# Performance work log

Measured on AMD Instinct MI355X. Metric: run time of the kernel, lower is better.

The kernel has to match this reference:

```python
import jax, jax.numpy as jnp
import numpy as np

B = 32768        # batch
S = 256          # subnet_num
H1, H2 = 10, 6   # subnet_arch
L2_SMOOTH = 1e-3
EPS = 1e-10


def setup_inputs() -> dict:
    key = jax.random.key(0)
    k = jax.random.split(key, 7)
    def glorot(kk, shape, fan_in, fan_out):
        return (jax.random.normal(kk, shape, jnp.float32)
                * np.float32(np.sqrt(2.0 / (fan_in + fan_out))))
    x = jax.random.normal(k[0], (B, S), jnp.float32)
    W1 = glorot(k[1], (S, 1, H1), 1, H1)
    b1 = jnp.zeros((S, H1), jnp.float32)
    W2 = glorot(k[2], (S, H1, H2), H1, H2)
    b2 = jnp.zeros((S, H2), jnp.float32)
    W3 = glorot(k[3], (S, H2, 1), H2, 1)
    b3 = jnp.zeros((S, 1), jnp.float32)
    return {"x": x, "W1": W1, "b1": b1, "W2": W2, "b2": b2, "W3": W3, "b3": b3}


def _mlp_scalar(xs, W1, b1, W2, b2, W3, b3):
    # xs: scalar input of one subnet for one sample
    h = jnp.tanh(xs * W1[0] + b1)   # [H1]
    h = jnp.tanh(h @ W2 + b2)       # [H2]
    return (h @ W3 + b3)[0]         # scalar


def _per_subnet(fn):
    # inner vmap over batch (x axis 0, params broadcast), outer over subnets
    inner = jax.vmap(fn, in_axes=(0, None, None, None, None, None, None))
    return jax.vmap(inner, in_axes=(1, 0, 0, 0, 0, 0, 0))  # -> [S, B]


def reference(x, W1, b1, W2, b2, W3, b3):
    out = _per_subnet(_mlp_scalar)(x, W1, b1, W2, b2, W3, b3)           # [S, B]
    d2f = jax.grad(jax.grad(_mlp_scalar))                               # Hessian diag (scalar input)
    g2 = _per_subnet(d2f)(x, W1, b1, W2, b2, W3, b3)                    # [S, B]
    # training-mode batch stats (population std, as tf.math.reduce_std)
    mean = jnp.mean(out, axis=1, keepdims=True)                         # [S, 1]
    std = jnp.maximum(jnp.std(out, axis=1, keepdims=True), EPS)         # [S, 1]
    out_bn = ((out - mean) / std).T                                     # [B, S]
    smooth_loss = L2_SMOOTH * jnp.sum(jnp.mean(g2 * g2, axis=1) / std[:, 0])
    return out_bn, smooth_loss
```

## Files before the change

kernel.cpp:

```cpp
#include <hip/hip_runtime.h>
#include <math.h>

#define B 32768
#define S 256
#define H1 10
#define H2 6
#define ROWS 512
#define CH (B / ROWS)
#define WPB 2
#define L2_SMOOTH 1e-3f
#define EPS 1e-10f

#define LSC 2.8853900817779268f
#define C2L 0.6931471805599453f
#define RLS 0.34657359027997264f

typedef __attribute__((ext_vector_type(2))) float v2f;

__device__ __forceinline__ int rfl_i(int x) { return __builtin_amdgcn_readfirstlane(x); }
__device__ __forceinline__ float rfl(float x) {
    return __int_as_float(__builtin_amdgcn_readfirstlane(__float_as_int(x)));
}

__device__ __forceinline__ void tanh_pair_s(float a_s, float& th, float& s2) {
    const float e = __builtin_amdgcn_exp2f(a_s);
    const float r = __builtin_amdgcn_rcpf(e + 1.0f);
    th = fmaf(-2.0f, r, 1.0f);
    s2 = (4.0f * r) * (1.0f - r);
}

__global__ __launch_bounds__(128, 2) void k1_mlp(
    const float* __restrict__ x,
    const float* __restrict__ W1, const float* __restrict__ b1,
    const float* __restrict__ W2, const float* __restrict__ b2,
    const float* __restrict__ W3, const float* __restrict__ b3,
    float* __restrict__ out,
    float* __restrict__ psum,
    float* __restrict__ psum2,
    float* __restrict__ pg2)
{
    const int t   = threadIdx.x;
    const int wid = blockIdx.x * WPB + rfl_i(t >> 6);
    const int l   = t & 63;
    const int s   = wid & (S - 1);
    const int c   = wid >> 8;

    float w1[H1], w1e[H1], b1e[H1], m2w1[H1];
#pragma unroll
    for (int i = 0; i < H1; ++i) {
        const float w = rfl(W1[s * H1 + i]);
        w1[i]   = w;
        w1e[i]  = w * LSC;
        m2w1[i] = -2.0f * w * w;
        b1e[i]  = rfl(b1[s * H1 + i]) * LSC;
        asm("" : "+v"(b1e[i]));
    }
    v2f w2p[H1][3];
#pragma unroll
    for (int i = 0; i < H1; ++i)
#pragma unroll
        for (int jp = 0; jp < 3; ++jp) {
            w2p[i][jp].x = rfl(W2[(s * H1 + i) * H2 + 2 * jp    ]) * LSC;
            w2p[i][jp].y = rfl(W2[(s * H1 + i) * H2 + 2 * jp + 1]) * LSC;
        }
    v2f b2p[3];
#pragma unroll
    for (int jp = 0; jp < 3; ++jp) {
        b2p[jp].x = rfl(b2[s * H2 + 2 * jp    ]) * LSC;
        b2p[jp].y = rfl(b2[s * H2 + 2 * jp + 1]) * LSC;
    }
    float w3s[H2], w3g[H2];
#pragma unroll
    for (int j = 0; j < H2; ++j) {
        const float w = rfl(W3[s * H2 + j]);
        w3s[j] = w;
        w3g[j] = w * RLS;
    }
    float bb3 = b3[s];
    asm("" : "+v"(bb3));

    const size_t base = (size_t)(c * ROWS) * S + s + (size_t)l * S;
    const float* px = x   + base;
    float*       po = out + base;

    float so = 0.0f, so2 = 0.0f, sg2 = 0.0f;

#pragma unroll 1
    for (int k = 0; k < ROWS / 128; ++k) {
        const float xA = px[(size_t)(k * 128)      * S];
        const float xB = px[(size_t)(k * 128 + 64) * S];

        v2f vA[3], vpA[3], vppA[3], vB[3], vpB[3], vppB[3];

        float hA, tA, hB, tB;
        {
            tanh_pair_s(fmaf(xA, w1e[0], b1e[0]), hA, tA);
            tanh_pair_s(fmaf(xB, w1e[0], b1e[0]), hB, tB);
            const float hpA = tA * w1[0], hppA = (hA * hpA) * m2w1[0];
            const float hpB = tB * w1[0], hppB = (hB * hpB) * m2w1[0];
#pragma unroll
            for (int jp = 0; jp < 3; ++jp) {
                vA[jp]   = hA   * w2p[0][jp] + b2p[jp];
                vpA[jp]  = hpA  * w2p[0][jp];
                vppA[jp] = hppA * w2p[0][jp];
                vB[jp]   = hB   * w2p[0][jp] + b2p[jp];
                vpB[jp]  = hpB  * w2p[0][jp];
                vppB[jp] = hppB * w2p[0][jp];
            }
        }
#pragma unroll
        for (int i = 1; i < H1; ++i) {
            tanh_pair_s(fmaf(xA, w1e[i], b1e[i]), hA, tA);
            tanh_pair_s(fmaf(xB, w1e[i], b1e[i]), hB, tB);
            const float hpA = tA * w1[i], hppA = (hA * hpA) * m2w1[i];
            const float hpB = tB * w1[i], hppB = (hB * hpB) * m2w1[i];
#pragma unroll
            for (int jp = 0; jp < 3; ++jp) {
                vA[jp]   = hA   * w2p[i][jp] + vA[jp];
                vpA[jp]  = hpA  * w2p[i][jp] + vpA[jp];
                vppA[jp] = hppA * w2p[i][jp] + vppA[jp];
                vB[jp]   = hB   * w2p[i][jp] + vB[jp];
                vpB[jp]  = hpB  * w2p[i][jp] + vpB[jp];
                vppB[jp] = hppB * w2p[i][jp] + vppB[jp];
            }
        }

        float oA = bb3, g2A = 0.0f, oB = bb3, g2B = 0.0f;
#pragma unroll
        for (int jp = 0; jp < 3; ++jp) {
            {   float g, tg; tanh_pair_s(vA[jp].x, g, tg);
                const float q = g * vpA[jp].x, cc = -C2L * q;
                const float gpp = tg * fmaf(cc, vpA[jp].x, vppA[jp].x);
                oA = fmaf(g, w3s[2*jp], oA); g2A = fmaf(w3g[2*jp], gpp, g2A); }
            {   float g, tg; tanh_pair_s(vA[jp].y, g, tg);
                const float q = g * vpA[jp].y, cc = -C2L * q;
                const float gpp = tg * fmaf(cc, vpA[jp].y, vppA[jp].y);
                oA = fmaf(g, w3s[2*jp+1], oA); g2A = fmaf(w3g[2*jp+1], gpp, g2A); }
            {   float g, tg; tanh_pair_s(vB[jp].x, g, tg);
                const float q = g * vpB[jp].x, cc = -C2L * q;
                const float gpp = tg * fmaf(cc, vpB[jp].x, vppB[jp].x);
                oB = fmaf(g, w3s[2*jp], oB); g2B = fmaf(w3g[2*jp], gpp, g2B); }
            {   float g, tg; tanh_pair_s(vB[jp].y, g, tg);
                const float q = g * vpB[jp].y, cc = -C2L * q;
                const float gpp = tg * fmaf(cc, vpB[jp].y, vppB[jp].y);
                oB = fmaf(g, w3s[2*jp+1], oB); g2B = fmaf(w3g[2*jp+1], gpp, g2B); }
        }

        po[(size_t)(k * 128)      * S] = oA;
        po[(size_t)(k * 128 + 64) * S] = oB;
        so += oA; so2 = fmaf(oA, oA, so2); sg2 = fmaf(g2A, g2A, sg2);
        so += oB; so2 = fmaf(oB, oB, so2); sg2 = fmaf(g2B, g2B, sg2);
    }

#pragma unroll
    for (int m = 1; m < 64; m <<= 1) {
        so  += __shfl_xor(so,  m, 64);
        so2 += __shfl_xor(so2, m, 64);
        sg2 += __shfl_xor(sg2, m, 64);
    }
    if (l == 0) {
        psum [s * CH + c] = so;
        psum2[s * CH + c] = so2;
        pg2  [s * CH + c] = sg2;
    }
}

__global__ __launch_bounds__(64) void k2_reduce(
    const float* __restrict__ psum, const float* __restrict__ psum2,
    const float* __restrict__ pg2,
    float* __restrict__ mean_arr, float* __restrict__ rstd_arr,
    float* __restrict__ smooth_arr)
{
    const int s = blockIdx.x;
    const int l = threadIdx.x;

    float a  = psum [s * CH + l];
    float b_ = psum2[s * CH + l];
    float cc = pg2  [s * CH + l];
#pragma unroll
    for (int m = 1; m < 64; m <<= 1) {
        a  += __shfl_xor(a,  m, 64);
        b_ += __shfl_xor(b_, m, 64);
        cc += __shfl_xor(cc, m, 64);
    }
    if (l == 0) {
        const float inv_b = 1.0f / (float)B;
        const float mean  = a * inv_b;
        float var = b_ * inv_b - mean * mean;
        var = fmaxf(var, 0.0f);
        const float stdv = fmaxf(sqrtf(var), EPS);
        const float rstd = 1.0f / stdv;
        mean_arr[s]   = mean;
        rstd_arr[s]   = rstd;
        smooth_arr[s] = (cc * inv_b) * rstd;
    }
}

#define K3_NORM_BLOCKS (B * S / (256 * 4))
__global__ __launch_bounds__(256) void k3_norm(
    float* __restrict__ out,
    const float* __restrict__ mean_arr, const float* __restrict__ rstd_arr,
    const float* __restrict__ smooth_arr)
{
    if ((int)blockIdx.x == K3_NORM_BLOCKS) {
        const int t = threadIdx.x;
        __shared__ float sa[256];
        sa[t] = smooth_arr[t];
        __syncthreads();
        for (int st = 128; st > 0; st >>= 1) {
            if (t < st) sa[t] += sa[t + st];
            __syncthreads();
        }
        if (t == 0) out[B * S] = L2_SMOOTH * sa[0];
        return;
    }

    const int i4   = (int)blockIdx.x * 256 + (int)threadIdx.x;
    const int base = i4 * 4;
    float4 v = *reinterpret_cast<float4*>(&out[base]);
    const int s0 = base & (S - 1);
    v.x = (v.x - mean_arr[s0 + 0]) * rstd_arr[s0 + 0];
    v.y = (v.y - mean_arr[s0 + 1]) * rstd_arr[s0 + 1];
    v.z = (v.z - mean_arr[s0 + 2]) * rstd_arr[s0 + 2];
    v.w = (v.w - mean_arr[s0 + 3]) * rstd_arr[s0 + 3];
    *reinterpret_cast<float4*>(&out[base]) = v;
}

extern "C" void kernel_launch(void* const* d_in, const int* in_sizes, int n_in,
                              void* d_out, int out_size, void* d_ws, size_t ws_size,
                              hipStream_t stream) {
    const float* x  = (const float*)d_in[0];
    const float* W1 = (const float*)d_in[1];
    const float* b1 = (const float*)d_in[2];
    const float* W2 = (const float*)d_in[3];
    const float* b2 = (const float*)d_in[4];
    const float* W3 = (const float*)d_in[5];
    const float* b3 = (const float*)d_in[6];
    float* out = (float*)d_out;

    float* psum   = (float*)d_ws;
    float* psum2  = psum  + S * CH;
    float* pg2    = psum2 + S * CH;
    float* meanA  = pg2   + S * CH;
    float* rstdA  = meanA + S;
    float* smooth = rstdA + S;

    k1_mlp<<<S * CH / WPB, 64 * WPB, 0, stream>>>(
        x, W1, b1, W2, b2, W3, b3, out, psum, psum2, pg2);
    k2_reduce<<<S, 64, 0, stream>>>(psum, psum2, pg2, meanA, rstdA, smooth);
    k3_norm<<<K3_NORM_BLOCKS + 1, 256, 0, stream>>>(out, meanA, rstdA, smooth);
}
```

Baseline: 122.6 us.

## Process one sample per iteration, raise occupancy and swizzle block order

The MLP kernel now evaluates one sample per loop iteration instead of two interleaved ones. This removes the duplicated register state and lets launch bounds rise from 128 threads with 2 blocks to 256 threads with 6 blocks. Block indices are swizzled so that neighbouring blocks spread across chunks and subnets, which changes the memory access pattern and how work maps to CUs. The cost is less instruction-level parallelism per wave, which the higher wave count is meant to hide.

```diff
diff --git a/kernel.cpp b/kernel.cpp
--- a/kernel.cpp
+++ b/kernel.cpp
@@ -7,7 +7,8 @@
 #define H2 6
 #define ROWS 512
 #define CH (B / ROWS)
-#define WPB 2
+#define WPB 4
+#define NBLK (S * CH / WPB)
 #define L2_SMOOTH 1e-3f
 #define EPS 1e-10f
 
@@ -29,7 +30,7 @@
     s2 = (4.0f * r) * (1.0f - r);
 }
 
-__global__ __launch_bounds__(128, 2) void k1_mlp(
+__global__ __launch_bounds__(256, 6) void k1_mlp(
     const float* __restrict__ x,
     const float* __restrict__ W1, const float* __restrict__ b1,
     const float* __restrict__ W2, const float* __restrict__ b2,
@@ -40,7 +41,9 @@
     float* __restrict__ pg2)
 {
     const int t   = threadIdx.x;
-    const int wid = blockIdx.x * WPB + rfl_i(t >> 6);
+    const int bid = (int)blockIdx.x;
+    const int swz = (bid & 7) * (NBLK / 8) + (bid >> 3);
+    const int wid = swz * WPB + rfl_i(t >> 6);
     const int l   = t & 63;
     const int s   = wid & (S - 1);
     const int c   = wid >> 8;
@@ -68,6 +71,8 @@
     for (int jp = 0; jp < 3; ++jp) {
         b2p[jp].x = rfl(b2[s * H2 + 2 * jp    ]) * LSC;
         b2p[jp].y = rfl(b2[s * H2 + 2 * jp + 1]) * LSC;
+        asm("" : "+v"(b2p[jp].x));
+        asm("" : "+v"(b2p[jp].y));
     }
     float w3s[H2], w3g[H2];
 #pragma unroll
@@ -79,77 +84,60 @@
     float bb3 = b3[s];
     asm("" : "+v"(bb3));
 
-    const size_t base = (size_t)(c * ROWS) * S + s + (size_t)l * S;
+    const size_t base = (size_t)(c * ROWS + l) * S + s;
     const float* px = x   + base;
     float*       po = out + base;
 
     float so = 0.0f, so2 = 0.0f, sg2 = 0.0f;
 
 #pragma unroll 1
-    for (int k = 0; k < ROWS / 128; ++k) {
-        const float xA = px[(size_t)(k * 128)      * S];
-        const float xB = px[(size_t)(k * 128 + 64) * S];
-
-        v2f vA[3], vpA[3], vppA[3], vB[3], vpB[3], vppB[3];
-
-        float hA, tA, hB, tB;
+    for (int k = 0; k < ROWS / 64; ++k) {
+        const float xs = px[(size_t)(k * 64) * S];
+
+        v2f v[3], vp[3], vpp[3];
         {
-            tanh_pair_s(fmaf(xA, w1e[0], b1e[0]), hA, tA);
-            tanh_pair_s(fmaf(xB, w1e[0], b1e[0]), hB, tB);
-            const float hpA = tA * w1[0], hppA = (hA * hpA) * m2w1[0];
-            const float hpB = tB * w1[0], hppB = (hB * hpB) * m2w1[0];
+            float h, tt;
+            tanh_pair_s(fmaf(xs, w1e[0], b1e[0]), h, tt);
+            const float hp  = tt * w1[0];
+            const float hpp = (h * hp) * m2w1[0];
 #pragma unroll
             for (int jp = 0; jp < 3; ++jp) {
-                vA[jp]   = hA   * w2p[0][jp] + b2p[jp];
-                vpA[jp]  = hpA  * w2p[0][jp];
-                vppA[jp] = hppA * w2p[0][jp];
-                vB[jp]   = hB   * w2p[0][jp] + b2p[jp];
-                vpB[jp]  = hpB  * w2p[0][jp];
-                vppB[jp] = hppB * w2p[0][jp];
+                v[jp]   = h   * w2p[0][jp] + b2p[jp];
+                vp[jp]  = hp  * w2p[0][jp];
+                vpp[jp] = hpp * w2p[0][jp];
             }
         }
 #pragma unroll
         for (int i = 1; i < H1; ++i) {
-            tanh_pair_s(fmaf(xA, w1e[i], b1e[i]), hA, tA);
-            tanh_pair_s(fmaf(xB, w1e[i], b1e[i]), hB, tB);
-            const float hpA = tA * w1[i], hppA = (hA * hpA) * m2w1[i];
-            const float hpB = tB * w1[i], hppB = (hB * hpB) * m2w1[i];
+            float h, tt;
+            tanh_pair_s(fmaf(xs, w1e[i], b1e[i]), h, tt);
+            const float hp  = tt * w1[i];
+            const float hpp = (h * hp) * m2w1[i];
 #pragma unroll
             for (int jp = 0; jp < 3; ++jp) {
-                vA[jp]   = hA   * w2p[i][jp] + vA[jp];
-                vpA[jp]  = hpA  * w2p[i][jp] + vpA[jp];
-                vppA[jp] = hppA * w2p[i][jp] + vppA[jp];
-                vB[jp]   = hB   * w2p[i][jp] + vB[jp];
-                vpB[jp]  = hpB  * w2p[i][jp] + vpB[jp];
-                vppB[jp] = hppB * w2p[i][jp] + vppB[jp];
+                v[jp]   = h   * w2p[i][jp] + v[jp];
+                vp[jp]  = hp  * w2p[i][jp] + vp[jp];
+                vpp[jp] = hpp * w2p[i][jp] + vpp[jp];
             }
         }
 
-        float oA = bb3, g2A = 0.0f, oB = bb3, g2B = 0.0f;
+        float o = bb3, g2 = 0.0f;
 #pragma unroll
         for (int jp = 0; jp < 3; ++jp) {
-            {   float g, tg; tanh_pair_s(vA[jp].x, g, tg);
-                const float q = g * vpA[jp].x, cc = -C2L * q;
-                const float gpp = tg * fmaf(cc, vpA[jp].x, vppA[jp].x);
-                oA = fmaf(g, w3s[2*jp], oA); g2A = fmaf(w3g[2*jp], gpp, g2A); }
-            {   float g, tg; tanh_pair_s(vA[jp].y, g, tg);
-                const float q = g * vpA[jp].y, cc = -C2L * q;
-                const float gpp = tg * fmaf(cc, vpA[jp].y, vppA[jp].y);
-                oA = fmaf(g, w3s[2*jp+1], oA); g2A = fmaf(w3g[2*jp+1], gpp, g2A); }
-            {   float g, tg; tanh_pair_s(vB[jp].x, g, tg);
-                const float q = g * vpB[jp].x, cc = -C2L * q;
-                const float gpp = tg * fmaf(cc, vpB[jp].x, vppB[jp].x);
-                oB = fmaf(g, w3s[2*jp], oB); g2B = fmaf(w3g[2*jp], gpp, g2B); }
-            {   float g, tg; tanh_pair_s(vB[jp].y, g, tg);
-                const float q = g * vpB[jp].y, cc = -C2L * q;
-                const float gpp = tg * fmaf(cc, vpB[jp].y, vppB[jp].y);
-                oB = fmaf(g, w3s[2*jp+1], oB); g2B = fmaf(w3g[2*jp+1], gpp, g2B); }
-        }
-
-        po[(size_t)(k * 128)      * S] = oA;
-        po[(size_t)(k * 128 + 64) * S] = oB;
-        so += oA; so2 = fmaf(oA, oA, so2); sg2 = fmaf(g2A, g2A, sg2);
-        so += oB; so2 = fmaf(oB, oB, so2); sg2 = fmaf(g2B, g2B, sg2);
+            {   float g, tg; tanh_pair_s(v[jp].x, g, tg);
+                const float cc  = -C2L * (g * vp[jp].x);
+                const float gpp = tg * fmaf(cc, vp[jp].x, vpp[jp].x);
+                o  = fmaf(g, w3s[2*jp],   o);
+                g2 = fmaf(w3g[2*jp], gpp, g2); }
+            {   float g, tg; tanh_pair_s(v[jp].y, g, tg);
+                const float cc  = -C2L * (g * vp[jp].y);
+                const float gpp = tg * fmaf(cc, vp[jp].y, vpp[jp].y);
+                o  = fmaf(g, w3s[2*jp+1],   o);
+                g2 = fmaf(w3g[2*jp+1], gpp, g2); }
+        }
+
+        po[(size_t)(k * 64) * S] = o;
+        so += o; so2 = fmaf(o, o, so2); sg2 = fmaf(g2, g2, sg2);
     }
 
 #pragma unroll
@@ -245,7 +233,7 @@
     float* rstdA  = meanA + S;
     float* smooth = rstdA + S;
 
-    k1_mlp<<<S * CH / WPB, 64 * WPB, 0, stream>>>(
+    k1_mlp<<<NBLK, 64 * WPB, 0, stream>>>(
         x, W1, b1, W2, b2, W3, b3, out, psum, psum2, pg2);
     k2_reduce<<<S, 64, 0, stream>>>(psum, psum2, pg2, meanA, rstdA, smooth);
     k3_norm<<<K3_NORM_BLOCKS + 1, 256, 0, stream>>>(out, meanA, rstdA, smooth);
```

Result: slower. 398.6 us (+225.1%).
